# Optimization experiments

Hardware: AMD Instinct MI355X
Metric: run time of the kernel (lower is better)

Reference implementation:

```python
import jax, jax.numpy as jnp
import numpy as np

K = 2            # top-k experts
SCALING = 16.0 / 16.0  # alpha / r


def setup_inputs() -> dict:
    key = jax.random.key(0)
    ks = jax.random.split(key, 7)
    B, T, D, O, E, R = 2, 4096, 2048, 2048, 8, 16
    return {
        "x": jax.random.normal(ks[0], (B, T, D), dtype=jnp.float32),
        "W": jax.random.normal(ks[1], (O, D), dtype=jnp.float32) * (1.0 / np.sqrt(D)),
        "b": jax.random.normal(ks[2], (O,), dtype=jnp.float32) * 0.02,
        "lora_A": jax.random.normal(ks[3], (E, R, D), dtype=jnp.float32) * (1.0 / np.sqrt(D)),
        "lora_B": jax.random.normal(ks[4], (E, O, R), dtype=jnp.float32) * 0.02,
        "gate_w": jax.random.normal(ks[5], (E, D), dtype=jnp.float32) * 0.02,
        "gate_b": jax.random.normal(ks[6], (E,), dtype=jnp.float32) * 0.02,
    }


def reference(x, W, b, lora_A, lora_B, gate_w, gate_b):
    orig_shape = x.shape
    D = orig_shape[-1]
    O = W.shape[0]
    x_flat = x.reshape(-1, D)                                  # [N, D]

    base = x_flat @ W.T + b                                    # [N, O]

    logits = x_flat @ gate_w.T + gate_b                        # [N, E] (eval: no noise)
    topk_logits, topk_idx = jax.lax.top_k(logits, K)           # [N, K]
    gates = jax.nn.softmax(topk_logits, axis=-1)               # [N, K]

    xA = jnp.einsum('nd,erd->ner', x_flat, lora_A)             # [N, E, R]
    delta_all = jnp.einsum('ner,eor->neo', xA, lora_B)         # [N, E, O]

    delta_topk = jnp.take_along_axis(delta_all, topk_idx[:, :, None], axis=1)  # [N, K, O]
    lora_update = jnp.sum(delta_topk * gates[:, :, None], axis=1)              # [N, O]

    out = base + SCALING * lora_update
    return out.reshape(*orig_shape[:-1], O)
```

## Files before the change

### kernel.cpp

```cpp
#include <hip/hip_runtime.h>
#include <hip/hip_bf16.h>
#include <stdint.h>

#define N_ROWS 8192
#define DIM    2048
#define OUTD   2048
#define NEXP   8
#define RNK    16
#define ZCOLS  128
#define KAUG   2176

typedef unsigned short u16;
typedef float  f32x4  __attribute__((ext_vector_type(4)));
typedef __bf16 bf16x8 __attribute__((ext_vector_type(8)));

__device__ __forceinline__ u16 f2bf(float f) {
  unsigned u = __float_as_uint(f);
  return (u16)((u + 0x7fffu + ((u >> 16) & 1u)) >> 16);
}

#define GLOAD(SRC, DST) __builtin_amdgcn_global_load_lds( \
    (__attribute__((address_space(1))) void*)(SRC), \
    (__attribute__((address_space(3))) void*)(DST), 16, 0, 0)

__global__ __launch_bounds__(256) void k2a_lora(
    const float* __restrict__ lA, u16* __restrict__ ab)
{
  const int t  = threadIdx.x;
  const int ar = blockIdx.x;
  const float* src = lA + (size_t)ar * DIM;
  u16* dst = ab + (size_t)ar * DIM;
  #pragma unroll
  for (int i = 0; i < 2; ++i) {
    int c = t * 4 + i * 1024;
    float4 v = *(const float4*)(src + c);
    ushort4 s; s.x = f2bf(v.x); s.y = f2bf(v.y); s.z = f2bf(v.z); s.w = f2bf(v.w);
    *(ushort4*)(dst + c) = s;
  }
}

__global__ __launch_bounds__(256) void kfw_fused(
    const float* __restrict__ x, const float* __restrict__ gw,
    const float* __restrict__ gb, const u16* __restrict__ ab,
    u16* __restrict__ xaug,
    const float* __restrict__ W, const float* __restrict__ lB,
    u16* __restrict__ waug)
{
  const int t = threadIdx.x;

  if (blockIdx.x >= 512) {
    const int o = blockIdx.x - 512;
    const float* wr = W + (size_t)o * DIM;
    u16* dst = waug + (size_t)o * KAUG;
    #pragma unroll
    for (int i = 0; i < 2; ++i) {
      int c = t * 4 + i * 1024;
      float4 v = *(const float4*)(wr + c);
      ushort4 s; s.x = f2bf(v.x); s.y = f2bf(v.y); s.z = f2bf(v.z); s.w = f2bf(v.w);
      *(ushort4*)(dst + c) = s;
    }
    if (t < ZCOLS) {
      int e = t >> 4, r = t & 15;
      dst[DIM + t] = f2bf(lB[((size_t)e * OUTD + o) * RNK + r]);
    }
    return;
  }

  __shared__ __align__(16) u16 la[2][8192];
  __shared__ __align__(16) u16 xb[2][1024];
  __shared__ float4 gates[16];

  const int wave = t >> 6;
  const int lane = t & 63;
  const int r    = t >> 4;
  const int q    = t & 15;
  const size_t row0 = (size_t)blockIdx.x * 16;

  int lrow[4], lsch[4];
  #pragma unroll
  for (int i = 0; i < 4; ++i) {
    const int g = t + i * 256;
    lrow[i] = g >> 3;
    lsch[i] = (g & 7) ^ (lrow[i] & 7);
  }

  auto lab_load = [&](int c, int i) -> uint4 {
    return *(const uint4*)((const char*)(ab + (size_t)lrow[i] * DIM + c * 64)
                           + lsch[i] * 16);
  };

  uint4 lab[4];
  #pragma unroll
  for (int i = 0; i < 4; ++i) lab[i] = lab_load(0, i);
  float4 xv, gwv[8];
  xv = *(const float4*)(x + (row0 + r) * DIM + q * 4);
  #pragma unroll
  for (int e = 0; e < NEXP; ++e)
    gwv[e] = *(const float4*)(gw + (size_t)e * DIM + q * 4);

  float ga[NEXP] = {};
  f32x4 acc[2] = {};
  const int nfA = 2 * wave, nfB = 2 * wave + 1;

  for (int c = 0; c < 32; ++c) {
    const int C0 = c * 64;
    uint4 labn[4]; float4 xvn, gwvn[8];
    if (c + 1 < 32) {
      #pragma unroll
      for (int i = 0; i < 4; ++i) labn[i] = lab_load(c + 1, i);
      xvn = *(const float4*)(x + (row0 + r) * DIM + C0 + 64 + q * 4);
      #pragma unroll
      for (int e = 0; e < NEXP; ++e)
        gwvn[e] = *(const float4*)(gw + (size_t)e * DIM + C0 + 64 + q * 4);
    }
    __builtin_amdgcn_sched_barrier(0);

    #pragma unroll
    for (int i = 0; i < 4; ++i)
      *(uint4*)((char*)la[c & 1] + (t + i * 256) * 16) = lab[i];
    ushort4 s; s.x = f2bf(xv.x); s.y = f2bf(xv.y); s.z = f2bf(xv.z); s.w = f2bf(xv.w);
    *(ushort4*)(xaug + (row0 + r) * KAUG + C0 + q * 4) = s;
    #pragma unroll
    for (int e = 0; e < NEXP; ++e)
      ga[e] += xv.x * gwv[e].x + xv.y * gwv[e].y + xv.z * gwv[e].z + xv.w * gwv[e].w;
    {
      const int ch = q >> 1;
      const int by = r * 128 + ((ch ^ (r & 7)) * 16) + (q & 1) * 8;
      *(ushort4*)((char*)xb[c & 1] + by) = s;
    }

    asm volatile("s_waitcnt lgkmcnt(0)" ::: "memory");
    __builtin_amdgcn_sched_barrier(0);
    __builtin_amdgcn_s_barrier();

    const char* laP = (const char*)la[c & 1];
    const char* xbP = (const char*)xb[c & 1];
    #pragma unroll
    for (int ks = 0; ks < 2; ++ks) {
      const int ra = lane & 15;
      const int pa = ((ks * 4 + (lane >> 4)) ^ (ra & 7)) * 16;
      bf16x8 avf = *(const bf16x8*)(xbP + ra * 128 + pa);
      const int rbA = (lane & 15) + 16 * nfA;
      const int rbB = (lane & 15) + 16 * nfB;
      bf16x8 bvA = *(const bf16x8*)(laP + rbA * 128 + (((ks * 4 + (lane >> 4)) ^ (rbA & 7)) * 16));
      bf16x8 bvB = *(const bf16x8*)(laP + rbB * 128 + (((ks * 4 + (lane >> 4)) ^ (rbB & 7)) * 16));
      acc[0] = __builtin_amdgcn_mfma_f32_16x16x32_bf16(avf, bvA, acc[0], 0, 0, 0);
      acc[1] = __builtin_amdgcn_mfma_f32_16x16x32_bf16(avf, bvB, acc[1], 0, 0, 0);
    }

    #pragma unroll
    for (int i = 0; i < 4; ++i) lab[i] = labn[i];
    xv = xvn;
    #pragma unroll
    for (int e = 0; e < NEXP; ++e) gwv[e] = gwvn[e];
  }

  #pragma unroll
  for (int e = 0; e < NEXP; ++e) {
    float v = ga[e];
    v += __shfl_xor(v, 1); v += __shfl_xor(v, 2);
    v += __shfl_xor(v, 4); v += __shfl_xor(v, 8);
    ga[e] = v + gb[e];
  }
  if (q == 0) {
    int e0 = 0; float m0 = ga[0];
    #pragma unroll
    for (int e = 1; e < NEXP; ++e) if (ga[e] > m0) { m0 = ga[e]; e0 = e; }
    int e1 = (e0 == 0) ? 1 : 0; float m1 = ga[e1];
    #pragma unroll
    for (int e = 0; e < NEXP; ++e) if (e != e0 && ga[e] > m1) { m1 = ga[e]; e1 = e; }
    float tt  = expf(m1 - m0);
    float inv = 1.f / (1.f + tt);
    float4 gg; gg.x = inv; gg.y = tt * inv;
    gg.z = __int_as_float(e0); gg.w = __int_as_float(e1);
    gates[r] = gg;
  }
  __syncthreads();

  #pragma unroll
  for (int nfl = 0; nfl < 2; ++nfl) {
    const int e = 2 * wave + nfl;
    const int n = e * 16 + (lane & 15);
    #pragma unroll
    for (int j = 0; j < 4; ++j) {
      const int m = (lane >> 4) * 4 + j;
      float4 gg = gates[m];
      const float g = (e == __float_as_int(gg.z)) ? gg.x
                    : ((e == __float_as_int(gg.w)) ? gg.y : 0.f);
      xaug[(row0 + m) * KAUG + DIM + n] = f2bf(acc[nfl][j] * g);
    }
  }
}

__global__ __launch_bounds__(512, 2) void gemm256_pipe(
    const u16* __restrict__ A, int lda,
    const u16* __restrict__ Bm, int ldb,
    int Ksz, int grid_n,
    float* __restrict__ outF, int ldo, const float* __restrict__ bias)
{
  __shared__ __align__(16) u16 smem[65536];

  const int tid  = threadIdx.x;
  const int wave = tid >> 6;
  const int lane = tid & 63;

  int bid = blockIdx.x;
  const int nwg = gridDim.x;
  if ((nwg & 7) == 0) {
    const int cpx = nwg >> 3;
    bid = (bid & 7) * cpx + (bid >> 3);
  }
  const int tm = bid / grid_n;
  const int tn = bid % grid_n;
  const size_t row0 = (size_t)tm * 256;
  const size_t col0 = (size_t)tn * 256;

  const int l3  = lane >> 3;
  const int sch = ((lane & 7) ^ l3) << 4;
  const char* aSrc = (const char*)(A  + (row0 + (size_t)(wave * 8 + l3)) * lda) + sch;
  const char* bSrc = (const char*)(Bm + (col0 + (size_t)(wave * 8 + l3)) * ldb) + sch;
  const size_t arst = (size_t)lda * 128;
  const size_t brst = (size_t)ldb * 128;
  char* ldsA = (char*)smem + wave * 1024;
  char* ldsB = (char*)smem + 65536 + wave * 1024;

  auto stage = [&](int tt) {
    const size_t ko = (size_t)tt * 128;
    const int    sb = (tt & 1) << 15;
    #pragma unroll
    for (int i = 0; i < 4; ++i)
      GLOAD(aSrc + ko + i * arst, ldsA + sb + i * 8192);
    #pragma unroll
    for (int i = 0; i < 4; ++i)
      GLOAD(bSrc + ko + i * brst, ldsB + sb + i * 8192);
  };

  const int wm = wave >> 2, wn = wave & 3;
  const int x0 = ((lane >> 4) ^ (lane & 7)) << 4;
  const int offA0 = wm * 16384 + (lane & 15) * 128 + x0;
  const int offB0 = wn * 8192  + (lane & 15) * 128 + x0;

  f32x4 acc[8][4] = {};

  const int nk = Ksz / 64;
  stage(0); stage(1);

  for (int t = 0; t < nk; ++t) {
    if (t + 1 < nk) asm volatile("s_waitcnt vmcnt(8)" ::: "memory");
    else            asm volatile("s_waitcnt vmcnt(0)" ::: "memory");
    __builtin_amdgcn_s_barrier();
    __builtin_amdgcn_sched_barrier(0);

    const char* sa = (const char*)smem + ((t & 1) << 15);
    const char* sb = (const char*)smem + 65536 + ((t & 1) << 15);

    bf16x8 av0[8], bv0[4], av1[8], bv1[4];
    #pragma unroll
    for (int mf = 0; mf < 8; ++mf) av0[mf] = *(const bf16x8*)(sa + offA0 + mf * 2048);
    #pragma unroll
    for (int nf = 0; nf < 4; ++nf) bv0[nf] = *(const bf16x8*)(sb + offB0 + nf * 2048);
    __builtin_amdgcn_s_setprio(1);
    #pragma unroll
    for (int mf = 0; mf < 8; ++mf)
      #pragma unroll
      for (int nf = 0; nf < 2; ++nf)
        acc[mf][nf] = __builtin_amdgcn_mfma_f32_16x16x32_bf16(
            av0[mf], bv0[nf], acc[mf][nf], 0, 0, 0);
    __builtin_amdgcn_s_setprio(0);
    #pragma unroll
    for (int mf = 0; mf < 8; ++mf) av1[mf] = *(const bf16x8*)(sa + (offA0 ^ 64) + mf * 2048);
    #pragma unroll
    for (int nf = 0; nf < 4; ++nf) bv1[nf] = *(const bf16x8*)(sb + (offB0 ^ 64) + nf * 2048);
    __builtin_amdgcn_s_setprio(1);
    #pragma unroll
    for (int mf = 0; mf < 8; ++mf)
      #pragma unroll
      for (int nf = 2; nf < 4; ++nf)
        acc[mf][nf] = __builtin_amdgcn_mfma_f32_16x16x32_bf16(
            av0[mf], bv0[nf], acc[mf][nf], 0, 0, 0);
    __builtin_amdgcn_s_setprio(0);
    asm volatile("s_waitcnt lgkmcnt(0)" ::: "memory");
    __builtin_amdgcn_s_barrier();
    __builtin_amdgcn_sched_barrier(0);
    if (t + 2 < nk) stage(t + 2);
    __builtin_amdgcn_s_setprio(1);
    #pragma unroll
    for (int mf = 0; mf < 8; ++mf)
      #pragma unroll
      for (int nf = 0; nf < 4; ++nf)
        acc[mf][nf] = __builtin_amdgcn_mfma_f32_16x16x32_bf16(
            av1[mf], bv1[nf], acc[mf][nf], 0, 0, 0);
    __builtin_amdgcn_s_setprio(0);
  }

  #pragma unroll
  for (int nf = 0; nf < 4; ++nf) {
    const size_t c = col0 + wn * 64 + nf * 16 + (lane & 15);
    const float bvv = bias[c];
    #pragma unroll
    for (int mf = 0; mf < 8; ++mf) {
      const size_t rb = row0 + wm * 128 + mf * 16 + ((lane >> 4) << 2);
      #pragma unroll
      for (int j = 0; j < 4; ++j)
        outF[(rb + j) * (size_t)ldo + c] = acc[mf][nf][j] + bvv;
    }
  }
}

extern "C" void kernel_launch(void* const* d_in, const int* in_sizes, int n_in,
                              void* d_out, int out_size, void* d_ws, size_t ws_size,
                              hipStream_t stream) {
  const float* x  = (const float*)d_in[0];
  const float* W  = (const float*)d_in[1];
  const float* b  = (const float*)d_in[2];
  const float* lA = (const float*)d_in[3];
  const float* lB = (const float*)d_in[4];
  const float* gw = (const float*)d_in[5];
  const float* gb = (const float*)d_in[6];
  float* out = (float*)d_out;

  u16* xaug = (u16*)d_ws;
  u16* waug = xaug + (size_t)N_ROWS * KAUG;
  u16* ab   = waug + (size_t)OUTD * KAUG;

  hipLaunchKernelGGL(k2a_lora, dim3(ZCOLS), dim3(256), 0, stream, lA, ab);
  hipLaunchKernelGGL(kfw_fused, dim3(512 + OUTD), dim3(256), 0, stream,
                     x, gw, gb, ab, xaug, W, lB, waug);
  hipLaunchKernelGGL(gemm256_pipe,
                     dim3((N_ROWS / 256) * (OUTD / 256)), dim3(512), 0, stream,
                     xaug, KAUG, waug, KAUG, KAUG, OUTD / 256,
                     out, OUTD, b);
}
```

Baseline: 117.3 us.

## Shrink GEMM tile to 256x128 with K-step 32 for higher occupancy

Replaces the 256x256 tile, K=64-per-stage GEMM with a 256x128 tile, K=32 stage kernel that uses 48KB of LDS and launch bounds allowing 4 blocks per CU. Each wave now computes a 64x64 sub-tile with 16 MFMAs per step, and the LDS swizzle and load mapping are redone to match. The aim is more concurrent waves to hide memory latency and more workgroups to balance across CUs. In exchange, arithmetic intensity per tile drops and barriers per unit of work double, which raises global and LDS traffic.

```diff
diff --git a/kernel.cpp b/kernel.cpp
--- a/kernel.cpp
+++ b/kernel.cpp
@@ -192,13 +192,13 @@
   }
 }
 
-__global__ __launch_bounds__(512, 2) void gemm256_pipe(
+__global__ __launch_bounds__(512, 4) void gemm_pipe2(
     const u16* __restrict__ A, int lda,
     const u16* __restrict__ Bm, int ldb,
     int Ksz, int grid_n,
     float* __restrict__ outF, int ldo, const float* __restrict__ bias)
 {
-  __shared__ __align__(16) u16 smem[65536];
+  __shared__ __align__(16) u16 smem[24576];
 
   const int tid  = threadIdx.x;
   const int wave = tid >> 6;
@@ -213,93 +213,80 @@
   const int tm = bid / grid_n;
   const int tn = bid % grid_n;
   const size_t row0 = (size_t)tm * 256;
-  const size_t col0 = (size_t)tn * 256;
-
-  const int l3  = lane >> 3;
-  const int sch = ((lane & 7) ^ l3) << 4;
-  const char* aSrc = (const char*)(A  + (row0 + (size_t)(wave * 8 + l3)) * lda) + sch;
-  const char* bSrc = (const char*)(Bm + (col0 + (size_t)(wave * 8 + l3)) * ldb) + sch;
-  const size_t arst = (size_t)lda * 128;
-  const size_t brst = (size_t)ldb * 128;
-  char* ldsA = (char*)smem + wave * 1024;
-  char* ldsB = (char*)smem + 65536 + wave * 1024;
+  const size_t col0 = (size_t)tn * 128;
+
+  int Ra0, ka0, Ra1, ka1;
+  {
+    int L0 = tid, L1 = tid + 512;
+    int j0 = L0 >> 3, c0 = (L0 & 7) ^ (j0 & 7);
+    int j1 = L1 >> 3, c1 = (L1 & 7) ^ (j1 & 7);
+    Ra0 = 2 * j0 + (c0 >> 2); ka0 = c0 & 3;
+    Ra1 = 2 * j1 + (c1 >> 2); ka1 = c1 & 3;
+  }
+  const char* aP0 = (const char*)(A  + (row0 + (size_t)Ra0) * lda) + ka0 * 16;
+  const char* aP1 = (const char*)(A  + (row0 + (size_t)Ra1) * lda) + ka1 * 16;
+  const char* bP0 = (const char*)(Bm + (col0 + (size_t)Ra0) * ldb) + ka0 * 16;
+  char* dA0 = (char*)smem + wave * 1024;
+  char* dA1 = (char*)smem + 8192 + wave * 1024;
+  char* dB0 = (char*)smem + 32768 + wave * 1024;
 
   auto stage = [&](int tt) {
-    const size_t ko = (size_t)tt * 128;
-    const int    sb = (tt & 1) << 15;
-    #pragma unroll
-    for (int i = 0; i < 4; ++i)
-      GLOAD(aSrc + ko + i * arst, ldsA + sb + i * 8192);
-    #pragma unroll
-    for (int i = 0; i < 4; ++i)
-      GLOAD(bSrc + ko + i * brst, ldsB + sb + i * 8192);
+    const size_t ko = (size_t)tt * 64;
+    const int sa = (tt & 1) * 16384;
+    const int sb = (tt & 1) * 8192;
+    GLOAD(aP0 + ko, dA0 + sa);
+    GLOAD(aP1 + ko, dA1 + sa);
+    GLOAD(bP0 + ko, dB0 + sb);
   };
 
-  const int wm = wave >> 2, wn = wave & 3;
-  const int x0 = ((lane >> 4) ^ (lane & 7)) << 4;
-  const int offA0 = wm * 16384 + (lane & 15) * 128 + x0;
-  const int offB0 = wn * 8192  + (lane & 15) * 128 + x0;
-
-  f32x4 acc[8][4] = {};
-
-  const int nk = Ksz / 64;
+  const int wm = wave >> 1, wn = wave & 1;
+  const int l15 = lane & 15, l16 = lane >> 4;
+  const int p   = (((l15 & 1) << 2) | l16) ^ ((l15 >> 1) & 7);
+  const int offA0 = wm * 4096 + (l15 >> 1) * 128 + p * 16;
+  const int offB0 = wn * 4096 + (l15 >> 1) * 128 + p * 16;
+
+  f32x4 acc[4][4] = {};
+
+  const int nk = Ksz / 32;
   stage(0); stage(1);
 
   for (int t = 0; t < nk; ++t) {
-    if (t + 1 < nk) asm volatile("s_waitcnt vmcnt(8)" ::: "memory");
+    if (t + 1 < nk) asm volatile("s_waitcnt vmcnt(3)" ::: "memory");
     else            asm volatile("s_waitcnt vmcnt(0)" ::: "memory");
     __builtin_amdgcn_s_barrier();
     __builtin_amdgcn_sched_barrier(0);
 
-    const char* sa = (const char*)smem + ((t & 1) << 15);
-    const char* sb = (const char*)smem + 65536 + ((t & 1) << 15);
-
-    bf16x8 av0[8], bv0[4], av1[8], bv1[4];
-    #pragma unroll
-    for (int mf = 0; mf < 8; ++mf) av0[mf] = *(const bf16x8*)(sa + offA0 + mf * 2048);
-    #pragma unroll
-    for (int nf = 0; nf < 4; ++nf) bv0[nf] = *(const bf16x8*)(sb + offB0 + nf * 2048);
+    const char* sa = (const char*)smem + (t & 1) * 16384;
+    const char* sb = (const char*)smem + 32768 + (t & 1) * 8192;
+
+    bf16x8 av[4], bv[4];
+    #pragma unroll
+    for (int mf = 0; mf < 4; ++mf) av[mf] = *(const bf16x8*)(sa + offA0 + mf * 1024);
+    #pragma unroll
+    for (int nf = 0; nf < 4; ++nf) bv[nf] = *(const bf16x8*)(sb + offB0 + nf * 1024);
+
     __builtin_amdgcn_s_setprio(1);
     #pragma unroll
-    for (int mf = 0; mf < 8; ++mf)
+    for (int mf = 0; mf < 4; ++mf)
       #pragma unroll
-      for (int nf = 0; nf < 2; ++nf)
+      for (int nf = 0; nf < 4; ++nf)
         acc[mf][nf] = __builtin_amdgcn_mfma_f32_16x16x32_bf16(
-            av0[mf], bv0[nf], acc[mf][nf], 0, 0, 0);
+            av[mf], bv[nf], acc[mf][nf], 0, 0, 0);
     __builtin_amdgcn_s_setprio(0);
-    #pragma unroll
-    for (int mf = 0; mf < 8; ++mf) av1[mf] = *(const bf16x8*)(sa + (offA0 ^ 64) + mf * 2048);
-    #pragma unroll
-    for (int nf = 0; nf < 4; ++nf) bv1[nf] = *(const bf16x8*)(sb + (offB0 ^ 64) + nf * 2048);
-    __builtin_amdgcn_s_setprio(1);
-    #pragma unroll
-    for (int mf = 0; mf < 8; ++mf)
-      #pragma unroll
-      for (int nf = 2; nf < 4; ++nf)
-        acc[mf][nf] = __builtin_amdgcn_mfma_f32_16x16x32_bf16(
-            av0[mf], bv0[nf], acc[mf][nf], 0, 0, 0);
-    __builtin_amdgcn_s_setprio(0);
+
     asm volatile("s_waitcnt lgkmcnt(0)" ::: "memory");
     __builtin_amdgcn_s_barrier();
     __builtin_amdgcn_sched_barrier(0);
     if (t + 2 < nk) stage(t + 2);
-    __builtin_amdgcn_s_setprio(1);
-    #pragma unroll
-    for (int mf = 0; mf < 8; ++mf)
-      #pragma unroll
-      for (int nf = 0; nf < 4; ++nf)
-        acc[mf][nf] = __builtin_amdgcn_mfma_f32_16x16x32_bf16(
-            av1[mf], bv1[nf], acc[mf][nf], 0, 0, 0);
-    __builtin_amdgcn_s_setprio(0);
   }
 
   #pragma unroll
   for (int nf = 0; nf < 4; ++nf) {
-    const size_t c = col0 + wn * 64 + nf * 16 + (lane & 15);
+    const size_t c = col0 + wn * 64 + nf * 16 + l15;
     const float bvv = bias[c];
     #pragma unroll
-    for (int mf = 0; mf < 8; ++mf) {
-      const size_t rb = row0 + wm * 128 + mf * 16 + ((lane >> 4) << 2);
+    for (int mf = 0; mf < 4; ++mf) {
+      const size_t rb = row0 + wm * 64 + mf * 16 + (l16 << 2);
       #pragma unroll
       for (int j = 0; j < 4; ++j)
         outF[(rb + j) * (size_t)ldo + c] = acc[mf][nf][j] + bvv;
@@ -326,8 +313,8 @@
   hipLaunchKernelGGL(k2a_lora, dim3(ZCOLS), dim3(256), 0, stream, lA, ab);
   hipLaunchKernelGGL(kfw_fused, dim3(512 + OUTD), dim3(256), 0, stream,
                      x, gw, gb, ab, xaug, W, lB, waug);
-  hipLaunchKernelGGL(gemm256_pipe,
-                     dim3((N_ROWS / 256) * (OUTD / 256)), dim3(512), 0, stream,
-                     xaug, KAUG, waug, KAUG, KAUG, OUTD / 256,
+  hipLaunchKernelGGL(gemm_pipe2,
+                     dim3((N_ROWS / 256) * (OUTD / 128)), dim3(512), 0, stream,
+                     xaug, KAUG, waug, KAUG, KAUG, OUTD / 128,
                      out, OUTD, b);
 }
```

Result: slower. 129.9 us (+10.8%).

## Load LoRA-A and x fragments directly from global into MFMA registers, drop LDS staging

Applied to the files above, without the earlier changes.

The x·A prep kernel no longer stages the bf16 LoRA-A tile and the x tile through double-buffered LDS with a per-chunk block barrier. Each wave now loads its MFMA operands straight from global memory: x is converted to bf16 in registers, and the gate dot products run on a separate x slice. This removes the LDS writes, the barriers and the explicit register prefetch. In exchange, x is read from global twice, the loads are less coalesced, and there is no software prefetch to hide latency.

```diff
diff --git a/kernel.cpp b/kernel.cpp
--- a/kernel.cpp
+++ b/kernel.cpp
@@ -17,6 +17,13 @@
 __device__ __forceinline__ u16 f2bf(float f) {
   unsigned u = __float_as_uint(f);
   return (u16)((u + 0x7fffu + ((u >> 16) & 1u)) >> 16);
+}
+
+__device__ __forceinline__ bf16x8 cvt8(float4 a, float4 b) {
+  union { u16 u[8]; bf16x8 v; } r;
+  r.u[0] = f2bf(a.x); r.u[1] = f2bf(a.y); r.u[2] = f2bf(a.z); r.u[3] = f2bf(a.w);
+  r.u[4] = f2bf(b.x); r.u[5] = f2bf(b.y); r.u[6] = f2bf(b.z); r.u[7] = f2bf(b.w);
+  return r.v;
 }
 
 #define GLOAD(SRC, DST) __builtin_amdgcn_global_load_lds( \
@@ -66,93 +73,55 @@
     return;
   }
 
-  __shared__ __align__(16) u16 la[2][8192];
-  __shared__ __align__(16) u16 xb[2][1024];
   __shared__ float4 gates[16];
 
   const int wave = t >> 6;
   const int lane = t & 63;
-  const int r    = t >> 4;
-  const int q    = t & 15;
+  const int l15  = lane & 15;
+  const int l16  = lane >> 4;
   const size_t row0 = (size_t)blockIdx.x * 16;
 
-  int lrow[4], lsch[4];
-  #pragma unroll
-  for (int i = 0; i < 4; ++i) {
-    const int g = t + i * 256;
-    lrow[i] = g >> 3;
-    lsch[i] = (g & 7) ^ (lrow[i] & 7);
-  }
-
-  auto lab_load = [&](int c, int i) -> uint4 {
-    return *(const uint4*)((const char*)(ab + (size_t)lrow[i] * DIM + c * 64)
-                           + lsch[i] * 16);
-  };
-
-  uint4 lab[4];
-  #pragma unroll
-  for (int i = 0; i < 4; ++i) lab[i] = lab_load(0, i);
-  float4 xv, gwv[8];
-  xv = *(const float4*)(x + (row0 + r) * DIM + q * 4);
-  #pragma unroll
-  for (int e = 0; e < NEXP; ++e)
-    gwv[e] = *(const float4*)(gw + (size_t)e * DIM + q * 4);
+  const int wr = 4 * wave + l16;
+  const float* xw = x  + (row0 + wr)  * DIM + l15 * 4;
+  const float* xa = x  + (row0 + l15) * DIM + l16 * 8;
+  const u16*   bA = ab + (size_t)(32 * wave + l15)      * DIM + l16 * 8;
+  const u16*   bB = ab + (size_t)(32 * wave + 16 + l15) * DIM + l16 * 8;
+  u16* xo = xaug + (row0 + wr) * KAUG + l15 * 4;
 
   float ga[NEXP] = {};
   f32x4 acc[2] = {};
-  const int nfA = 2 * wave, nfB = 2 * wave + 1;
 
   for (int c = 0; c < 32; ++c) {
     const int C0 = c * 64;
-    uint4 labn[4]; float4 xvn, gwvn[8];
-    if (c + 1 < 32) {
-      #pragma unroll
-      for (int i = 0; i < 4; ++i) labn[i] = lab_load(c + 1, i);
-      xvn = *(const float4*)(x + (row0 + r) * DIM + C0 + 64 + q * 4);
-      #pragma unroll
-      for (int e = 0; e < NEXP; ++e)
-        gwvn[e] = *(const float4*)(gw + (size_t)e * DIM + C0 + 64 + q * 4);
-    }
-    __builtin_amdgcn_sched_barrier(0);
-
-    #pragma unroll
-    for (int i = 0; i < 4; ++i)
-      *(uint4*)((char*)la[c & 1] + (t + i * 256) * 16) = lab[i];
-    ushort4 s; s.x = f2bf(xv.x); s.y = f2bf(xv.y); s.z = f2bf(xv.z); s.w = f2bf(xv.w);
-    *(ushort4*)(xaug + (row0 + r) * KAUG + C0 + q * 4) = s;
+    float4 wv = *(const float4*)(xw + C0);
+    float4 af[2][2];
+    #pragma unroll
+    for (int ks = 0; ks < 2; ++ks) {
+      af[ks][0] = *(const float4*)(xa + C0 + ks * 32);
+      af[ks][1] = *(const float4*)(xa + C0 + ks * 32 + 4);
+    }
+    bf16x8 bva[2], bvb[2];
+    #pragma unroll
+    for (int ks = 0; ks < 2; ++ks) {
+      bva[ks] = *(const bf16x8*)(bA + C0 + ks * 32);
+      bvb[ks] = *(const bf16x8*)(bB + C0 + ks * 32);
+    }
+    float4 gv4[NEXP];
     #pragma unroll
     for (int e = 0; e < NEXP; ++e)
-      ga[e] += xv.x * gwv[e].x + xv.y * gwv[e].y + xv.z * gwv[e].z + xv.w * gwv[e].w;
-    {
-      const int ch = q >> 1;
-      const int by = r * 128 + ((ch ^ (r & 7)) * 16) + (q & 1) * 8;
-      *(ushort4*)((char*)xb[c & 1] + by) = s;
-    }
-
-    asm volatile("s_waitcnt lgkmcnt(0)" ::: "memory");
-    __builtin_amdgcn_sched_barrier(0);
-    __builtin_amdgcn_s_barrier();
-
-    const char* laP = (const char*)la[c & 1];
-    const char* xbP = (const char*)xb[c & 1];
+      gv4[e] = *(const float4*)(gw + (size_t)e * DIM + C0 + l15 * 4);
+
+    ushort4 s; s.x = f2bf(wv.x); s.y = f2bf(wv.y); s.z = f2bf(wv.z); s.w = f2bf(wv.w);
+    *(ushort4*)(xo + C0) = s;
+    #pragma unroll
+    for (int e = 0; e < NEXP; ++e)
+      ga[e] += wv.x * gv4[e].x + wv.y * gv4[e].y + wv.z * gv4[e].z + wv.w * gv4[e].w;
     #pragma unroll
     for (int ks = 0; ks < 2; ++ks) {
-      const int ra = lane & 15;
-      const int pa = ((ks * 4 + (lane >> 4)) ^ (ra & 7)) * 16;
-      bf16x8 avf = *(const bf16x8*)(xbP + ra * 128 + pa);
-      const int rbA = (lane & 15) + 16 * nfA;
-      const int rbB = (lane & 15) + 16 * nfB;
-      bf16x8 bvA = *(const bf16x8*)(laP + rbA * 128 + (((ks * 4 + (lane >> 4)) ^ (rbA & 7)) * 16));
-      bf16x8 bvB = *(const bf16x8*)(laP + rbB * 128 + (((ks * 4 + (lane >> 4)) ^ (rbB & 7)) * 16));
-      acc[0] = __builtin_amdgcn_mfma_f32_16x16x32_bf16(avf, bvA, acc[0], 0, 0, 0);
-      acc[1] = __builtin_amdgcn_mfma_f32_16x16x32_bf16(avf, bvB, acc[1], 0, 0, 0);
-    }
-
-    #pragma unroll
-    for (int i = 0; i < 4; ++i) lab[i] = labn[i];
-    xv = xvn;
-    #pragma unroll
-    for (int e = 0; e < NEXP; ++e) gwv[e] = gwvn[e];
+      bf16x8 av = cvt8(af[ks][0], af[ks][1]);
+      acc[0] = __builtin_amdgcn_mfma_f32_16x16x32_bf16(av, bva[ks], acc[0], 0, 0, 0);
+      acc[1] = __builtin_amdgcn_mfma_f32_16x16x32_bf16(av, bvb[ks], acc[1], 0, 0, 0);
+    }
   }
 
   #pragma unroll
@@ -162,7 +131,7 @@
     v += __shfl_xor(v, 4); v += __shfl_xor(v, 8);
     ga[e] = v + gb[e];
   }
-  if (q == 0) {
+  if (l15 == 0) {
     int e0 = 0; float m0 = ga[0];
     #pragma unroll
     for (int e = 1; e < NEXP; ++e) if (ga[e] > m0) { m0 = ga[e]; e0 = e; }
@@ -173,17 +142,17 @@
     float inv = 1.f / (1.f + tt);
     float4 gg; gg.x = inv; gg.y = tt * inv;
     gg.z = __int_as_float(e0); gg.w = __int_as_float(e1);
-    gates[r] = gg;
+    gates[wr] = gg;
   }
   __syncthreads();
 
   #pragma unroll
   for (int nfl = 0; nfl < 2; ++nfl) {
     const int e = 2 * wave + nfl;
-    const int n = e * 16 + (lane & 15);
+    const int n = e * 16 + l15;
     #pragma unroll
     for (int j = 0; j < 4; ++j) {
-      const int m = (lane >> 4) * 4 + j;
+      const int m = l16 * 4 + j;
       float4 gg = gates[m];
       const float g = (e == __float_as_int(gg.z)) ? gg.x
                     : ((e == __float_as_int(gg.w)) ? gg.y : 0.f);
```

New measurement: 151.8 us. +29.4%, slower.
